# Optimization experiments

Measured on AMD Instinct MI355X. Metric: run time of the kernel, lower is better.

Reference implementation:

```python
import jax, jax.numpy as jnp
import numpy as np

B, T, D, V, L = 32, 512, 512, 1024, 128
BLANK = 0
NEG = -1e30  # log-domain 'minus infinity' that is fp-safe


def setup_inputs() -> dict:
    key = jax.random.key(0)
    k1, k2, k3 = jax.random.split(key, 3)
    x = jax.random.normal(k1, (B, T, D), dtype=jnp.float32)
    W = jax.random.normal(k2, (D, V), dtype=jnp.float32) / np.sqrt(D).astype(np.float32)
    b = jnp.zeros((V,), dtype=jnp.float32)
    # CTC targets must be in [1, V) (never the blank id 0)
    target = jax.random.randint(k3, (B, L), 1, V)
    input_lengths = jnp.full((B,), T, dtype=jnp.int32)
    target_lengths = jnp.full((B,), L, dtype=jnp.int32)
    return {"x": x, "W": W, "b": b, "target": target,
            "input_lengths": input_lengths, "target_lengths": target_lengths}


def _ctc_loss(log_probs, target, input_lengths, target_lengths):
    # log_probs: [T, B, V] (time-major), target: [B, L]
    Tt, Bb, _ = log_probs.shape
    Ll = target.shape[1]
    S = 2 * Ll + 1  # extended label sequence: blank,t0,blank,t1,...,blank
    ext = jnp.full((Bb, S), BLANK, dtype=target.dtype).at[:, 1::2].set(target)  # [B,S]
    ext_m2 = jnp.pad(ext, ((0, 0), (2, 0)), constant_values=BLANK)[:, :S]
    skip = (ext != BLANK) & (ext != ext_m2) & (jnp.arange(S)[None, :] >= 2)  # [B,S]

    # gather log-probs of extended labels for every time step: [T,B,S]
    lp_ext = jnp.take_along_axis(log_probs, jnp.broadcast_to(ext[None], (Tt, Bb, S)), axis=2)

    alpha0 = jnp.full((Bb, S), NEG, log_probs.dtype)
    alpha0 = alpha0.at[:, 0].set(lp_ext[0, :, 0]).at[:, 1].set(lp_ext[0, :, 1])

    def step(alpha, lp_t):
        a1 = jnp.pad(alpha, ((0, 0), (1, 0)), constant_values=NEG)[:, :S]
        a2 = jnp.pad(alpha, ((0, 0), (2, 0)), constant_values=NEG)[:, :S]
        c = jnp.logaddexp(alpha, a1)
        c = jnp.where(skip, jnp.logaddexp(c, a2), c)
        new = c + lp_t
        return new, new

    _, alphas = jax.lax.scan(step, alpha0, lp_ext[1:])
    alphas = jnp.concatenate([alpha0[None], alphas], axis=0)  # [T,B,S]

    bi = jnp.arange(Bb)
    a_last = alphas[input_lengths - 1, bi]  # [B,S] alpha at each sample's final frame
    ll = jnp.logaddexp(a_last[bi, 2 * target_lengths - 1], a_last[bi, 2 * target_lengths])
    nll = -ll  # per-sample negative log-likelihood
    # zero_infinity=True: infinite losses are zeroed
    nll = jnp.where(jnp.isinf(nll) | (nll > 1e29), 0.0, nll)
    # reduction='mean': divide each loss by its target length, then mean
    return jnp.mean(nll / jnp.maximum(target_lengths, 1).astype(nll.dtype))


def reference(x, W, b, target, input_lengths, target_lengths):
    logits = jnp.einsum('btd,dv->btv', x, W) + b  # nn.Linear
    log_probs = jax.nn.log_softmax(logits, axis=-1)  # [B,T,V]
    return _ctc_loss(jnp.transpose(log_probs, (1, 0, 2)), target, input_lengths, target_lengths)
```

## Files before the change

kernel.cpp:

```cpp
#include <hip/hip_runtime.h>
#include <cstdint>


#define PROW 256
#define PEXT_PAD_ROWS 64
#define L2E 1.4426950408889634f
#define LN2 0.6931471805599453f

typedef short v8s __attribute__((ext_vector_type(8)));
typedef float v4f __attribute__((ext_vector_type(4)));

__device__ __forceinline__ uint32_t f2bf_bits(float f) {
  uint32_t u = __float_as_uint(f);
  return (u + 0x7FFFu + ((u >> 16) & 1u)) >> 16;
}
__device__ __forceinline__ float bf2f(uint32_t h) { return __uint_as_float(h << 16); }

__global__ void k_prep(const float* __restrict__ x, uint16_t* __restrict__ xb, long long n,
                       const float* __restrict__ W, uint16_t* __restrict__ Wt, int D, int V,
                       float* __restrict__ out, int nconv) {
  if (blockIdx.x == 0 && threadIdx.x == 0) out[0] = 0.f;
  if ((int)blockIdx.x < nconv) {
    long long i = ((long long)blockIdx.x * blockDim.x + threadIdx.x) * 8;
    if (i >= n) return;
    float4 a = *(const float4*)(x + i);
    float4 b = *(const float4*)(x + i + 4);
    uint4 o;
    o.x = f2bf_bits(a.x) | (f2bf_bits(a.y) << 16);
    o.y = f2bf_bits(a.z) | (f2bf_bits(a.w) << 16);
    o.z = f2bf_bits(b.x) | (f2bf_bits(b.y) << 16);
    o.w = f2bf_bits(b.z) | (f2bf_bits(b.w) << 16);
    *(uint4*)(xb + i) = o;
  } else {
    __shared__ float tile[32][33];
    const int bid2 = blockIdx.x - nconv;
    const int n0 = (bid2 % (V / 32)) * 32, k0 = (bid2 / (V / 32)) * 32;
    const int tx = threadIdx.x & 31, ty = threadIdx.x >> 5;
    #pragma unroll
    for (int i = 0; i < 32; i += 8)
      tile[ty + i][tx] = W[(size_t)(k0 + ty + i) * V + n0 + tx];
    __syncthreads();
    #pragma unroll
    for (int i = 0; i < 32; i += 8)
      Wt[(size_t)(n0 + ty + i) * D + k0 + tx] = (uint16_t)f2bf_bits(tile[tx][ty + i]);
  }
}

__global__ __launch_bounds__(256) void k_gemm(const uint16_t* __restrict__ A,
                                              const uint16_t* __restrict__ Bt,
                                              const float* __restrict__ bias,
                                              uint16_t* __restrict__ C, int M, int N, int K) {
  __shared__ uint16_t As[2][128 * 32];
  __shared__ uint16_t Bs[2][128 * 32];
  const int tid = threadIdx.x, lane = tid & 63, wave = tid >> 6;
  int d = blockIdx.x;
  const int nwg = gridDim.x;
  if ((nwg & 7) == 0) d = (d & 7) * (nwg >> 3) + (d >> 3);
  const int ntl = N >> 7;
  const int m0 = (d / ntl) * 128, n0 = (d % ntl) * 128;
  const int wm = wave & 1, wn = wave >> 1;
  const int frow = lane & 15, kb = lane >> 4;
  const int lr = lane >> 2, kc = lane & 3;
  v4f acc[4][4] = {};

  for (int k0 = 0; k0 < K; k0 += 64) {
    __syncthreads();
    #pragma unroll
    for (int t = 0; t < 2; t++)
      #pragma unroll
      for (int i = 0; i < 2; i++) {
        const int r = (wave * 2 + i) * 16 + lr;
        const uint16_t* ga = A + (size_t)(m0 + r) * K + k0 + t * 32 + kc * 8;
        const uint16_t* gb = Bt + (size_t)(n0 + r) * K + k0 + t * 32 + kc * 8;
        __builtin_amdgcn_global_load_lds(
            (const __attribute__((address_space(1))) void*)ga,
            (__attribute__((address_space(3))) void*)(&As[t][0] + (wave * 2 + i) * 512 + lane * 8), 16, 0, 0);
        __builtin_amdgcn_global_load_lds(
            (const __attribute__((address_space(1))) void*)gb,
            (__attribute__((address_space(3))) void*)(&Bs[t][0] + (wave * 2 + i) * 512 + lane * 8), 16, 0, 0);
      }
    __syncthreads();

    #pragma unroll
    for (int t = 0; t < 2; t++) {
      v8s af[4], bf[4];
      #pragma unroll
      for (int i = 0; i < 4; i++)
        af[i] = *(const v8s*)(&As[t][0] + (wm * 64 + i * 16 + frow) * 32 + kb * 8);
      #pragma unroll
      for (int j = 0; j < 4; j++)
        bf[j] = *(const v8s*)(&Bs[t][0] + (wn * 64 + j * 16 + frow) * 32 + kb * 8);
      #pragma unroll
      for (int i = 0; i < 4; i++)
        #pragma unroll
        for (int j = 0; j < 4; j++)
          acc[i][j] = __builtin_amdgcn_mfma_f32_16x16x32_bf16(af[i], bf[j], acc[i][j], 0, 0, 0);
    }
  }

  const int crow = (lane >> 4) * 4, ccol = lane & 15;
  #pragma unroll
  for (int j = 0; j < 4; j++) {
    const int n = n0 + wn * 64 + j * 16 + ccol;
    const float bv = bias[n];
    #pragma unroll
    for (int i = 0; i < 4; i++) {
      const int mb = m0 + wm * 64 + i * 16 + crow;
      #pragma unroll
      for (int r2 = 0; r2 < 4; r2++)
        C[(size_t)(mb + r2) * N + n] = (uint16_t)f2bf_bits(acc[i][j][r2] + bv);
    }
  }
}

__global__ void k_softmax_gather(const uint16_t* __restrict__ logits, const int* __restrict__ target,
                                 const int* __restrict__ tlen, float* __restrict__ pext,
                                 int T, int V, int L) {
  const int row = blockIdx.x * 4 + (threadIdx.x >> 6);
  const int lane = threadIdx.x & 63;
  const uint16_t* lrow = logits + (size_t)row * V;

  float xs[16];
  int cnt = 0;
  float mx = -INFINITY;
  for (int base = 0; base < V; base += 256) {
    const int idx = base + lane * 4;
    uint2 u = *(const uint2*)(lrow + idx);
    float4 v;
    v.x = bf2f(u.x & 0xFFFFu); v.y = bf2f(u.x >> 16);
    v.z = bf2f(u.y & 0xFFFFu); v.w = bf2f(u.y >> 16);
    xs[cnt] = v.x; xs[cnt + 1] = v.y; xs[cnt + 2] = v.z; xs[cnt + 3] = v.w; cnt += 4;
    mx = fmaxf(mx, fmaxf(fmaxf(v.x, v.y), fmaxf(v.z, v.w)));
  }
  #pragma unroll
  for (int off = 32; off; off >>= 1) mx = fmaxf(mx, __shfl_xor(mx, off, 64));
  float sum = 0.f;
  #pragma unroll
  for (int q = 0; q < 16; q++) { if (q < cnt) sum += exp2f((xs[q] - mx) * L2E); }
  #pragma unroll
  for (int off = 32; off; off >>= 1) sum += __shfl_xor(sum, off, 64);
  const float lse2 = mx * L2E + log2f(sum);

  const int bidx = row / T;
  const int Lb = tlen[bidx];
  const int S = 2 * Lb + 1;
  float* prow = pext + (size_t)row * PROW;
  #pragma unroll
  for (int it = 0; it < PROW / 64; it++) {
    const int s = lane + it * 64;
    float p = 0.f;
    if (s < S) {
      const int lbl = (s & 1) ? target[bidx * L + ((s - 1) >> 1)] : 0;
      p = exp2f(bf2f(lrow[lbl]) * L2E - lse2);
    }
    prow[s] = p;
  }
}

__device__ __forceinline__ float wave_shr1(float x) {
  return __int_as_float(__builtin_amdgcn_update_dpp(0, __float_as_int(x), 0x138, 0xf, 0xf, true));
}
__device__ __forceinline__ float wave_max_nonneg(float x) {
  x = fmaxf(x, __int_as_float(__builtin_amdgcn_update_dpp(0, __float_as_int(x), 0x111, 0xf, 0xf, true)));
  x = fmaxf(x, __int_as_float(__builtin_amdgcn_update_dpp(0, __float_as_int(x), 0x112, 0xf, 0xf, true)));
  x = fmaxf(x, __int_as_float(__builtin_amdgcn_update_dpp(0, __float_as_int(x), 0x114, 0xf, 0xf, true)));
  x = fmaxf(x, __int_as_float(__builtin_amdgcn_update_dpp(0, __float_as_int(x), 0x118, 0xf, 0xf, true)));
  x = fmaxf(x, __int_as_float(__builtin_amdgcn_update_dpp(0, __float_as_int(x), 0x142, 0xf, 0xf, true)));
  x = fmaxf(x, __int_as_float(__builtin_amdgcn_update_dpp(0, __float_as_int(x), 0x143, 0xf, 0xf, true)));
  return __int_as_float(__builtin_amdgcn_readlane(__float_as_int(x), 63));
}

__device__ __forceinline__ void load8(float4* __restrict__ p,
                                      const float* __restrict__ pb, int t0, int lane) {
  #pragma unroll
  for (int k = 0; k < 8; k++)
    p[k] = *(const float4*)(pb + (size_t)(t0 + k) * PROW + (lane << 2));
}

__global__ __launch_bounds__(64, 1) void k_ctc(const float* __restrict__ pext,
                                               const int* __restrict__ target,
                                               const int* __restrict__ ilen,
                                               const int* __restrict__ tlen,
                                               float* __restrict__ out, int T, int L) {
  const int b = blockIdx.x;
  const int lane = threadIdx.x;
  const int B = gridDim.x;
  const int Tb = ilen[b];
  const int Lb = tlen[b];
  const int S = 2 * Lb + 1;
  const int* tg = target + b * L;

  const int s1 = 4 * lane + 1, s3 = 4 * lane + 3;
  float sk1 = 0.f, sk3 = 0.f;
  if (s1 >= 3 && s1 < S) sk1 = (tg[(s1 - 1) >> 1] != tg[(s1 - 3) >> 1]) ? 1.f : 0.f;
  if (s3 >= 3 && s3 < S) sk3 = (tg[(s3 - 1) >> 1] != tg[(s3 - 3) >> 1]) ? 1.f : 0.f;

  const float* pb = pext + (size_t)b * T * PROW;
  const float4 p0 = *(const float4*)(pb + (lane << 2));
  float a0 = (lane == 0) ? p0.x : 0.f;
  float a1 = (lane == 0) ? p0.y : 0.f;
  float a2 = 0.f, a3 = 0.f, a4 = 0.f;
  float log2C = 0.f;

  #define CTC_STEP(PP) {                                                \
    const float pm3 = wave_shr1(a3);                                    \
    const float a255 = __int_as_float(__builtin_amdgcn_readlane(__float_as_int(a3), 63)); \
    const float p4v = __int_as_float(__builtin_amdgcn_readlane(__float_as_int((PP).x), 0)); \
    const float n0v = (a0 + pm3) * (PP).x;                              \
    const float n1v = (a1 + a0 + sk1 * pm3) * (PP).y;                   \
    const float n2v = (a2 + a1) * (PP).z;                               \
    const float n3v = (a3 + a2 + sk3 * a1) * (PP).w;                    \
    const float n4v = (a4 + a255) * p4v;                                \
    a0 = n0v; a1 = n1v; a2 = n2v; a3 = n3v; a4 = n4v; }

  #define RENORM {                                                      \
    float m = fmaxf(fmaxf(fmaxf(a0, a1), fmaxf(a2, a3)), a4);           \
    m = wave_max_nonneg(m);                                             \
    const int e = (int)((__float_as_uint(m) >> 23) & 255u) - 127;       \
    const float scale = __uint_as_float((uint32_t)(127 - e) << 23);     \
    a0 *= scale; a1 *= scale; a2 *= scale; a3 *= scale; a4 *= scale;    \
    log2C += (float)e; }

  float4 Pa[8], Pb_[8], Pc[8], Pd[8];
  int t0 = 1;
  bool done = false;
  load8(Pa, pb, t0, lane);
  load8(Pb_, pb, t0 + 8, lane);
  load8(Pc, pb, t0 + 16, lane);
  __builtin_amdgcn_sched_barrier(0);

  #define PHASE(LP, CP) {                                               \
    if (t0 + 8 <= Tb) {                                                 \
      load8(LP, pb, t0 + 24, lane);                                     \
      __builtin_amdgcn_sched_barrier(0);                                \
      _Pragma("unroll")                                                 \
      for (int k = 0; k < 8; k++) CTC_STEP(CP[k]);                      \
      RENORM; t0 += 8;                                                  \
    } else {                                                            \
      _Pragma("unroll")                                                 \
      for (int k = 0; k < 8; k++) { if (t0 + k < Tb) CTC_STEP(CP[k]); } \
      RENORM; done = true;                                              \
    } }

  while (!done) {
    PHASE(Pd, Pa); if (done) break;
    PHASE(Pa, Pb_); if (done) break;
    PHASE(Pb_, Pc); if (done) break;
    PHASE(Pc, Pd);
  }

  __shared__ float abuf[257];
  abuf[4 * lane + 0] = a0; abuf[4 * lane + 1] = a1;
  abuf[4 * lane + 2] = a2; abuf[4 * lane + 3] = a3;
  if (lane == 63) abuf[256] = a4;
  __syncthreads();
  if (lane == 0) {
    const float ssum = abuf[2 * Lb - 1] + abuf[2 * Lb];
    const float ll = (log2f(ssum) + log2C) * LN2;
    float nll = -ll;
    if (!(nll < 1e29f)) nll = 0.f;
    atomicAdd(out, nll / ((float)(Lb > 0 ? Lb : 1) * (float)B));
  }
}

extern "C" void kernel_launch(void* const* d_in, const int* in_sizes, int n_in,
                              void* d_out, int out_size, void* d_ws, size_t ws_size,
                              hipStream_t stream) {
  const float* x      = (const float*)d_in[0];
  const float* W      = (const float*)d_in[1];
  const float* bias   = (const float*)d_in[2];
  const int*  target  = (const int*)d_in[3];
  const int*  ilen    = (const int*)d_in[4];
  const int*  tlen    = (const int*)d_in[5];

  const int B = in_sizes[4];
  const int V = in_sizes[2];
  const int D = in_sizes[1] / V;
  const int T = in_sizes[0] / (B * D);
  const int L = in_sizes[3] / B;
  const int M = B * T;

  char* ws = (char*)d_ws;
  const size_t xb_bytes = (size_t)M * D * 2;
  const size_t wt_bytes = (size_t)V * D * 2;
  uint16_t* xb = (uint16_t*)ws;
  uint16_t* Wt = (uint16_t*)(ws + xb_bytes);
  uint16_t* logits = (uint16_t*)(ws + xb_bytes + wt_bytes);
  const size_t log_bytes = (size_t)M * V * 2;

  const size_t pext_bytes = (size_t)(M + PEXT_PAD_ROWS) * PROW * 4;
  float* pext;
  if (pext_bytes <= xb_bytes + wt_bytes) {
    pext = (float*)ws;
  } else {
    pext = (float*)(ws + xb_bytes + wt_bytes + log_bytes);
  }

  const long long nx = (long long)M * D;
  const int nconv = (int)((nx / 8 + 255) / 256);
  const int ntrans = (V / 32) * (D / 32);
  k_prep<<<nconv + ntrans, 256, 0, stream>>>(x, xb, nx, W, Wt, D, V, (float*)d_out, nconv);
  k_gemm<<<(M / 128) * (V / 128), 256, 0, stream>>>(xb, Wt, bias, logits, M, V, D);
  k_softmax_gather<<<M / 4, 256, 0, stream>>>(logits, target, tlen, pext, T, V, L);
  k_ctc<<<B, 64, 0, stream>>>(pext, target, ilen, tlen, (float*)d_out, T, L);
}
```

Baseline: 160.2 us.

## Split CTC kernel into producer waves staging probabilities through LDS ring

The CTC recurrence kernel now launches 256 threads per sample. Wave 0 runs the alpha recursion, reading 8-timestep chunks from a double-buffered shared-memory ring. Waves 1-3 take turns prefetching chunks from global memory and writing them into the ring. This replaces the single wave's register-held global prefetch pipeline, aiming to hide global load latency from the serial recurrence, at the cost of a workgroup barrier every chunk plus LDS round-trips.

```diff
diff --git a/kernel.cpp b/kernel.cpp
--- a/kernel.cpp
+++ b/kernel.cpp
@@ -170,93 +170,130 @@
   return __int_as_float(__builtin_amdgcn_readlane(__float_as_int(x), 63));
 }
 
-__device__ __forceinline__ void load8(float4* __restrict__ p,
-                                      const float* __restrict__ pb, int t0, int lane) {
+__device__ __forceinline__ void load8r(float4* __restrict__ p,
+                                       const float* __restrict__ pb, int t0, int lane) {
   #pragma unroll
   for (int k = 0; k < 8; k++)
     p[k] = *(const float4*)(pb + (size_t)(t0 + k) * PROW + (lane << 2));
 }
 
-__global__ __launch_bounds__(64, 1) void k_ctc(const float* __restrict__ pext,
-                                               const int* __restrict__ target,
-                                               const int* __restrict__ ilen,
-                                               const int* __restrict__ tlen,
-                                               float* __restrict__ out, int T, int L) {
+__global__ __launch_bounds__(256, 1) void k_ctc(const float* __restrict__ pext,
+                                                const int* __restrict__ target,
+                                                const int* __restrict__ ilen,
+                                                const int* __restrict__ tlen,
+                                                float* __restrict__ out, int T, int L) {
+  __shared__ __attribute__((aligned(16))) float ring[2][8][PROW];
+  __shared__ float abuf[257];
+  __shared__ float lc_sh;
+
   const int b = blockIdx.x;
-  const int lane = threadIdx.x;
+  const int tid = threadIdx.x;
+  const int lane = tid & 63, wave = tid >> 6;
   const int B = gridDim.x;
   const int Tb = ilen[b];
   const int Lb = tlen[b];
   const int S = 2 * Lb + 1;
   const int* tg = target + b * L;
-
-  const int s1 = 4 * lane + 1, s3 = 4 * lane + 3;
-  float sk1 = 0.f, sk3 = 0.f;
-  if (s1 >= 3 && s1 < S) sk1 = (tg[(s1 - 1) >> 1] != tg[(s1 - 3) >> 1]) ? 1.f : 0.f;
-  if (s3 >= 3 && s3 < S) sk3 = (tg[(s3 - 1) >> 1] != tg[(s3 - 3) >> 1]) ? 1.f : 0.f;
-
   const float* pb = pext + (size_t)b * T * PROW;
-  const float4 p0 = *(const float4*)(pb + (lane << 2));
-  float a0 = (lane == 0) ? p0.x : 0.f;
-  float a1 = (lane == 0) ? p0.y : 0.f;
-  float a2 = 0.f, a3 = 0.f, a4 = 0.f;
-  float log2C = 0.f;
-
-  #define CTC_STEP(PP) {                                                \
-    const float pm3 = wave_shr1(a3);                                    \
-    const float a255 = __int_as_float(__builtin_amdgcn_readlane(__float_as_int(a3), 63)); \
-    const float p4v = __int_as_float(__builtin_amdgcn_readlane(__float_as_int((PP).x), 0)); \
-    const float n0v = (a0 + pm3) * (PP).x;                              \
-    const float n1v = (a1 + a0 + sk1 * pm3) * (PP).y;                   \
-    const float n2v = (a2 + a1) * (PP).z;                               \
-    const float n3v = (a3 + a2 + sk3 * a1) * (PP).w;                    \
-    const float n4v = (a4 + a255) * p4v;                                \
-    a0 = n0v; a1 = n1v; a2 = n2v; a3 = n3v; a4 = n4v; }
-
-  #define RENORM {                                                      \
-    float m = fmaxf(fmaxf(fmaxf(a0, a1), fmaxf(a2, a3)), a4);           \
-    m = wave_max_nonneg(m);                                             \
-    const int e = (int)((__float_as_uint(m) >> 23) & 255u) - 127;       \
-    const float scale = __uint_as_float((uint32_t)(127 - e) << 23);     \
-    a0 *= scale; a1 *= scale; a2 *= scale; a3 *= scale; a4 *= scale;    \
-    log2C += (float)e; }
-
-  float4 Pa[8], Pb_[8], Pc[8], Pd[8];
-  int t0 = 1;
-  bool done = false;
-  load8(Pa, pb, t0, lane);
-  load8(Pb_, pb, t0 + 8, lane);
-  load8(Pc, pb, t0 + 16, lane);
-  __builtin_amdgcn_sched_barrier(0);
-
-  #define PHASE(LP, CP) {                                               \
-    if (t0 + 8 <= Tb) {                                                 \
-      load8(LP, pb, t0 + 24, lane);                                     \
-      __builtin_amdgcn_sched_barrier(0);                                \
-      _Pragma("unroll")                                                 \
-      for (int k = 0; k < 8; k++) CTC_STEP(CP[k]);                      \
-      RENORM; t0 += 8;                                                  \
-    } else {                                                            \
-      _Pragma("unroll")                                                 \
-      for (int k = 0; k < 8; k++) { if (t0 + k < Tb) CTC_STEP(CP[k]); } \
-      RENORM; done = true;                                              \
-    } }
-
-  while (!done) {
-    PHASE(Pd, Pa); if (done) break;
-    PHASE(Pa, Pb_); if (done) break;
-    PHASE(Pb_, Pc); if (done) break;
-    PHASE(Pc, Pd);
-  }
-
-  __shared__ float abuf[257];
-  abuf[4 * lane + 0] = a0; abuf[4 * lane + 1] = a1;
-  abuf[4 * lane + 2] = a2; abuf[4 * lane + 3] = a3;
-  if (lane == 63) abuf[256] = a4;
+  const int CT = (Tb + 6) >> 3;
+
+  if (wave == 0) {
+    const int s1 = 4 * lane + 1, s3 = 4 * lane + 3;
+    float sk1 = 0.f, sk3 = 0.f;
+    if (s1 >= 3 && s1 < S) sk1 = (tg[(s1 - 1) >> 1] != tg[(s1 - 3) >> 1]) ? 1.f : 0.f;
+    if (s3 >= 3 && s3 < S) sk3 = (tg[(s3 - 1) >> 1] != tg[(s3 - 3) >> 1]) ? 1.f : 0.f;
+
+    const float4 p0 = *(const float4*)(pb + (lane << 2));
+    float a0 = (lane == 0) ? p0.x : 0.f;
+    float a1 = (lane == 0) ? p0.y : 0.f;
+    float a2 = 0.f, a3 = 0.f, a4 = 0.f;
+    float log2C = 0.f;
+
+    #define CTC_STEP(PP) {                                                \
+      const float pm3 = wave_shr1(a3);                                    \
+      const float a255 = __int_as_float(__builtin_amdgcn_readlane(__float_as_int(a3), 63)); \
+      const float p4v = __int_as_float(__builtin_amdgcn_readlane(__float_as_int((PP).x), 0)); \
+      const float n0v = (a0 + pm3) * (PP).x;                              \
+      const float n1v = (a1 + a0 + sk1 * pm3) * (PP).y;                   \
+      const float n2v = (a2 + a1) * (PP).z;                               \
+      const float n3v = (a3 + a2 + sk3 * a1) * (PP).w;                    \
+      const float n4v = (a4 + a255) * p4v;                                \
+      a0 = n0v; a1 = n1v; a2 = n2v; a3 = n3v; a4 = n4v; }
+
+    #define RENORM {                                                      \
+      float m = fmaxf(fmaxf(fmaxf(a0, a1), fmaxf(a2, a3)), a4);           \
+      m = wave_max_nonneg(m);                                             \
+      const int e = (int)((__float_as_uint(m) >> 23) & 255u) - 127;       \
+      const float scale = __uint_as_float((uint32_t)(127 - e) << 23);     \
+      a0 *= scale; a1 *= scale; a2 *= scale; a3 *= scale; a4 *= scale;    \
+      log2C += (float)e; }
+
+    asm volatile("" ::: "memory");
+    __builtin_amdgcn_s_barrier();
+    asm volatile("" ::: "memory");
+
+    for (int c = 0; c < CT; ++c) {
+      const int slot = c & 1;
+      float4 P[8];
+      #pragma unroll
+      for (int k = 0; k < 8; ++k)
+        P[k] = *(const float4*)(&ring[slot][k][lane << 2]);
+      const int t0 = 1 + 8 * c;
+      if (t0 + 8 <= Tb) {
+        #pragma unroll
+        for (int k = 0; k < 8; ++k) CTC_STEP(P[k]);
+        RENORM;
+      } else {
+        #pragma unroll
+        for (int k = 0; k < 8; ++k) { if (t0 + k < Tb) CTC_STEP(P[k]); }
+        RENORM;
+      }
+      asm volatile("" ::: "memory");
+      __builtin_amdgcn_s_barrier();
+      asm volatile("" ::: "memory");
+    }
+
+    abuf[4 * lane + 0] = a0; abuf[4 * lane + 1] = a1;
+    abuf[4 * lane + 2] = a2; abuf[4 * lane + 3] = a3;
+    if (lane == 63) abuf[256] = a4;
+    if (lane == 0) lc_sh = log2C;
+  } else {
+    const int p = wave;
+    float4 buf[8];
+    const int c0 = p - 1;
+    if (c0 < CT) load8r(buf, pb, 1 + 8 * c0, lane);
+    if (p == 1 && 0 < CT) {
+      #pragma unroll
+      for (int k = 0; k < 8; ++k)
+        *(float4*)(&ring[0][k][lane << 2]) = buf[k];
+      if (3 < CT) load8r(buf, pb, 1 + 8 * 3, lane);
+      asm volatile("s_waitcnt lgkmcnt(0)" ::: "memory");
+    }
+    asm volatile("" ::: "memory");
+    __builtin_amdgcn_s_barrier();
+    asm volatile("" ::: "memory");
+
+    for (int c = 0; c < CT; ++c) {
+      const int cpub = c + 1;
+      if (cpub < CT && (cpub % 3) == p - 1) {
+        const int slot = cpub & 1;
+        #pragma unroll
+        for (int k = 0; k < 8; ++k)
+          *(float4*)(&ring[slot][k][lane << 2]) = buf[k];
+        const int cnext = cpub + 3;
+        if (cnext < CT) load8r(buf, pb, 1 + 8 * cnext, lane);
+        asm volatile("s_waitcnt lgkmcnt(0)" ::: "memory");
+      }
+      asm volatile("" ::: "memory");
+      __builtin_amdgcn_s_barrier();
+      asm volatile("" ::: "memory");
+    }
+  }
+
   __syncthreads();
-  if (lane == 0) {
+  if (tid == 0) {
     const float ssum = abuf[2 * Lb - 1] + abuf[2 * Lb];
-    const float ll = (log2f(ssum) + log2C) * LN2;
+    const float ll = (log2f(ssum) + lc_sh) * LN2;
     float nll = -ll;
     if (!(nll < 1e29f)) nll = 0.f;
     atomicAdd(out, nll / ((float)(Lb > 0 ? Lb : 1) * (float)B));
@@ -302,5 +339,5 @@
   k_prep<<<nconv + ntrans, 256, 0, stream>>>(x, xb, nx, W, Wt, D, V, (float*)d_out, nconv);
   k_gemm<<<(M / 128) * (V / 128), 256, 0, stream>>>(xb, Wt, bias, logits, M, V, D);
   k_softmax_gather<<<M / 4, 256, 0, stream>>>(logits, target, tlen, pext, T, V, L);
-  k_ctc<<<B, 64, 0, stream>>>(pext, target, ilen, tlen, (float*)d_out, T, L);
-}
+  k_ctc<<<B, 256, 0, stream>>>(pext, target, ilen, tlen, (float*)d_out, T, L);
+}
```

New measurement: 182.3 us. 13.8% more time.
